# Performance work log

Measured on AMD Instinct MI355X. Metric: run time of the kernel, lower is better.

The kernel has to match this reference:

```python
import jax, jax.numpy as jnp
import numpy as np


def setup_inputs() -> dict:
    key = jax.random.key(0)
    k0, k1, k2, k3 = jax.random.split(key, 4)
    B, T, D, F, E = 4, 2048, 512, 1024, 8
    x = jax.random.normal(k0, (B, T, D), dtype=jnp.float32)
    # router weight is zero-init in the original; use small random values so top-k
    router_w = 0.02 * jax.random.normal(k1, (E, D), dtype=jnp.float32)
    router_b = jnp.zeros((E,), dtype=jnp.float32)
    w_gate_up = 0.02 * jax.random.normal(k2, (E, D, 2 * F), dtype=jnp.float32)
    w_down = 0.02 * jax.random.normal(k3, (E, F, D), dtype=jnp.float32)
    return {"x": x, "router_w": router_w, "router_b": router_b,
            "w_gate_up": w_gate_up, "w_down": w_down, "top_k": 2}


def reference(x, router_w, router_b, w_gate_up, w_down, top_k):
    B, T, D = x.shape
    E = router_w.shape[0]
    x_flat = x.reshape(-1, D)                      # [N, D]
    N = x_flat.shape[0]

    # router: softmax over experts, top-k, renormalize
    logits = x_flat @ router_w.T + router_b       # [N, E]
    probs = jax.nn.softmax(logits, axis=-1)
    top_w, top_idx = jax.lax.top_k(probs, top_k)  # [N, k]
    top_w = top_w / jnp.sum(top_w, axis=-1, keepdims=True)

    # scatter renormalized weights into a dense [N, E] combine matrix
    combine = jnp.zeros((N, E), dtype=x.dtype).at[
        jnp.arange(N)[:, None], top_idx].add(top_w)

    # per-expert SwiGLU; combine weights zero out non-selected experts, giving
    # math identical to the sort/gather/scatter dispatch in the original
    out = jnp.zeros_like(x_flat)
    for e in range(E):  # fixed small expert count, not a data-dim loop
        gate_up = x_flat @ w_gate_up[e]           # [N, 2F]
        gate, up = jnp.split(gate_up, 2, axis=-1)
        h = jax.nn.silu(gate) * up                # [N, F]
        out = out + combine[:, e:e + 1] * (h @ w_down[e])
    return out.reshape(B, T, D)
```

## Files before the change

kernel.cpp:

```cpp
#include <hip/hip_runtime.h>
#include <stdint.h>

#define N_TOK 8192
#define D_DIM 512
#define F_DIM 1024
#define E_NUM 8
#define M_SLOTS (N_TOK * 2)

typedef __bf16 bf16x8 __attribute__((ext_vector_type(8)));
typedef float f32x4 __attribute__((ext_vector_type(4)));

__device__ __forceinline__ ushort f2b(float f) {
    union { float f; unsigned u; } v; v.f = f;
    unsigned r = v.u + 0x7fffu + ((v.u >> 16) & 1u);
    return (ushort)(r >> 16);
}
__device__ __forceinline__ float b2f(ushort u) {
    union { unsigned i; float f; } v; v.i = ((unsigned)u) << 16; return v.f;
}
__device__ __forceinline__ void gload16(const void* g, void* l) {
    __builtin_amdgcn_global_load_lds(
        (const __attribute__((address_space(1))) unsigned int*)g,
        (__attribute__((address_space(3))) unsigned int*)l, 16, 0, 0);
}

__global__ __launch_bounds__(256) void transpose_all_k(const float* __restrict__ wgu,
                                                       ushort* __restrict__ wgu_t,
                                                       const float* __restrict__ wd,
                                                       ushort* __restrict__ wd_t) {
    __shared__ ushort tile[64][65];
    int b = blockIdx.x;
    const float* src; ushort* dst; int R, C, c0, r0;
    if (b < 2048) {
        int e = b >> 8, rem = b & 255;
        R = D_DIM; C = 2 * F_DIM;
        src = wgu + (size_t)e * R * C; dst = wgu_t + (size_t)e * R * C;
        c0 = (rem & 31) * 64; r0 = (rem >> 5) * 64;
    } else {
        int b2 = b - 2048;
        int e = b2 >> 7, rem = b2 & 127;
        R = F_DIM; C = D_DIM;
        src = wd + (size_t)e * R * C; dst = wd_t + (size_t)e * R * C;
        c0 = (rem & 7) * 64; r0 = (rem >> 3) * 64;
    }
#pragma unroll
    for (int i = 0; i < 4; ++i) {
        int ch = threadIdx.x + i * 256;
        int row = ch >> 4, pos = ch & 15;
        float4 v = *(const float4*)(src + (size_t)(r0 + row) * C + c0 + pos * 4);
        tile[row][pos * 4 + 0] = f2b(v.x);
        tile[row][pos * 4 + 1] = f2b(v.y);
        tile[row][pos * 4 + 2] = f2b(v.z);
        tile[row][pos * 4 + 3] = f2b(v.w);
    }
    __syncthreads();
#pragma unroll
    for (int i = 0; i < 2; ++i) {
        int ch = threadIdx.x + i * 256;
        int ocol = ch >> 3, rb = ch & 7;
        ushort tmp[8];
#pragma unroll
        for (int j = 0; j < 8; ++j) tmp[j] = tile[rb * 8 + j][ocol];
        *(uint4*)(dst + (size_t)(c0 + ocol) * R + r0 + rb * 8) = *(const uint4*)tmp;
    }
}

__global__ __launch_bounds__(256) void logits_k(const float* __restrict__ x,
                                                const float* __restrict__ rw,
                                                const float* __restrict__ rb,
                                                ushort* __restrict__ x_bf,
                                                int* __restrict__ tok_e,
                                                float* __restrict__ tok_w) {
    int lane = threadIdx.x & 63, wv = threadIdx.x >> 6;
    int t = blockIdx.x * 4 + wv;
    float4 xa = *(const float4*)(x + (size_t)t * D_DIM + lane * 8);
    float4 xb = *(const float4*)(x + (size_t)t * D_DIM + lane * 8 + 4);
    ushort u[8] = {f2b(xa.x), f2b(xa.y), f2b(xa.z), f2b(xa.w),
                   f2b(xb.x), f2b(xb.y), f2b(xb.z), f2b(xb.w)};
    *(uint4*)(x_bf + (size_t)t * D_DIM + lane * 8) = *(const uint4*)u;

    float acc[E_NUM];
#pragma unroll
    for (int e = 0; e < E_NUM; ++e) {
        float4 wa = *(const float4*)(rw + (size_t)e * D_DIM + lane * 8);
        float4 wb = *(const float4*)(rw + (size_t)e * D_DIM + lane * 8 + 4);
        float s = xa.x * wa.x + xa.y * wa.y + xa.z * wa.z + xa.w * wa.w +
                  xb.x * wb.x + xb.y * wb.y + xb.z * wb.z + xb.w * wb.w;
#pragma unroll
        for (int o = 32; o > 0; o >>= 1) s += __shfl_xor(s, o, 64);
        acc[e] = s;
    }
    if (lane == 0) {
        float l[E_NUM];
#pragma unroll
        for (int e = 0; e < E_NUM; ++e) l[e] = acc[e] + rb[e];
        int e0 = 0;
#pragma unroll
        for (int e = 1; e < E_NUM; ++e) if (l[e] > l[e0]) e0 = e;
        int e1 = (e0 == 0) ? 1 : 0;
#pragma unroll
        for (int e = 0; e < E_NUM; ++e) if (e != e0 && l[e] > l[e1]) e1 = e;
        float p1 = __expf(l[e1] - l[e0]);
        float w0 = 1.f / (1.f + p1), w1 = p1 / (1.f + p1);
        tok_e[2 * t] = e0;  tok_e[2 * t + 1] = e1;
        tok_w[2 * t] = w0;  tok_w[2 * t + 1] = w1;
    }
}

__global__ __launch_bounds__(1024) void route_k(const int* __restrict__ tok_e,
                                                int* __restrict__ ebase,
                                                int* __restrict__ row_token,
                                                int* __restrict__ tok_pos) {
    __shared__ int lcnt[E_NUM];
    __shared__ int base_s[E_NUM];
    int tid = threadIdx.x, lane = tid & 63;
    if (tid < E_NUM) lcnt[tid] = 0;
    __syncthreads();
    int ev[16], intra[16];
#pragma unroll
    for (int j = 0; j < 16; ++j) {
        int i = tid + j * 1024;
        int e = tok_e[i];
        unsigned long long m = ~0ull;
#pragma unroll
        for (int b = 0; b < 3; ++b) {
            unsigned long long vb = __ballot(((e >> b) & 1) != 0);
            m &= ((e >> b) & 1) ? vb : ~vb;
        }
        int prefix = __popcll(m & ((1ull << lane) - 1ull));
        int leader = __ffsll((unsigned long long)m) - 1;
        int bs = 0;
        if (lane == leader) bs = atomicAdd(&lcnt[e], __popcll(m));
        bs = __shfl(bs, leader, 64);
        ev[j] = e; intra[j] = bs + prefix;
    }
    __syncthreads();
    if (tid == 0) {
        int s = 0;
        for (int k = 0; k < E_NUM; ++k) { base_s[k] = s; ebase[k] = s; s += lcnt[k]; }
        ebase[E_NUM] = s;
    }
    __syncthreads();
#pragma unroll
    for (int j = 0; j < 16; ++j) {
        int i = tid + j * 1024;
        int pos = base_s[ev[j]] + intra[j];
        row_token[pos] = i >> 1;
        tok_pos[i] = pos;
    }
}

__global__ __launch_bounds__(256, 3) void gemm1_k(const ushort* __restrict__ x,
                                                  const ushort* __restrict__ wgu_t,
                                                  const int* __restrict__ ebase,
                                                  const int* __restrict__ row_token,
                                                  ushort* __restrict__ h) {
    int e = blockIdx.z;
    int base = ebase[e];
    int cnt = ebase[e + 1] - base;
    int tile0 = blockIdx.y * 128;
    if (tile0 >= cnt) return;
    int c0 = blockIdx.x * 64;

    __shared__ __align__(16) ushort smem[3 * 8192];

    int tid = threadIdx.x;
    int lane = tid & 63, wv = tid >> 6;
    int wr = wv >> 1, wc = wv & 1;

    const ushort* asrc[2];
    const ushort* bsrc[2];
#pragma unroll
    for (int i = 0; i < 2; ++i) {
        int c = tid + i * 256;
        int rp = c >> 3, s = c & 7;
        int lp = s ^ (rp & 7);
        int row = 2 * rp + (lp >> 2);
        int q = lp & 3;
        int r = tile0 + row;
        r = (r < cnt) ? r : (cnt - 1);
        int tok = row_token[base + r];
        asrc[i] = x + (size_t)tok * D_DIM + q * 8;
        int gc = (row < 64) ? (c0 + row) : (F_DIM + c0 + row - 64);
        bsrc[i] = wgu_t + ((size_t)e * (2 * F_DIM) + gc) * D_DIM + q * 8;
    }

    f32x4 accg[4][2], accu[4][2];
#pragma unroll
    for (int a = 0; a < 4; ++a)
#pragma unroll
        for (int b = 0; b < 2; ++b) {
            accg[a][b] = (f32x4){0.f, 0.f, 0.f, 0.f};
            accu[a][b] = (f32x4){0.f, 0.f, 0.f, 0.f};
        }

    int q = lane >> 4, m = lane & 15;
    int mh = m >> 1;
    int sl = (4 * (m & 1) + q) ^ (mh & 7);
    int soff = sl * 8;

    auto stage = [&](ushort* buf, int kk) {
#pragma unroll
        for (int i = 0; i < 2; ++i) {
            int c = tid + i * 256;
            gload16(asrc[i] + kk, buf + (size_t)c * 8);
            gload16(bsrc[i] + kk, buf + 4096 + (size_t)c * 8);
        }
    };
    auto compute = [&](const ushort* la_) {
        const ushort* lb_ = la_ + 4096;
        bf16x8 af[4], bg[2], bu[2];
#pragma unroll
        for (int mt = 0; mt < 4; ++mt)
            af[mt] = *(const bf16x8*)(la_ + (wr * 32 + mt * 8 + mh) * 64 + soff);
#pragma unroll
        for (int nt = 0; nt < 2; ++nt) {
            bg[nt] = *(const bf16x8*)(lb_ + (wc * 16 + nt * 8 + mh) * 64 + soff);
            bu[nt] = *(const bf16x8*)(lb_ + (32 + wc * 16 + nt * 8 + mh) * 64 + soff);
        }
#pragma unroll
        for (int mt = 0; mt < 4; ++mt)
#pragma unroll
            for (int nt = 0; nt < 2; ++nt) {
                accg[mt][nt] = __builtin_amdgcn_mfma_f32_16x16x32_bf16(af[mt], bg[nt], accg[mt][nt], 0, 0, 0);
                accu[mt][nt] = __builtin_amdgcn_mfma_f32_16x16x32_bf16(af[mt], bu[nt], accu[mt][nt], 0, 0, 0);
            }
    };

    ushort* pc = smem;
    ushort* pn = smem + 8192;
    ushort* pf = smem + 16384;

    stage(pc, 0);
    stage(pn, 32);
    asm volatile("s_waitcnt vmcnt(4) lgkmcnt(0)" ::: "memory");
    __builtin_amdgcn_s_barrier();
    __builtin_amdgcn_sched_barrier(0);

    for (int k = 64; k <= D_DIM - 32; k += 32) {
        stage(pf, k);
        compute(pc);
        asm volatile("s_waitcnt vmcnt(4) lgkmcnt(0)" ::: "memory");
        __builtin_amdgcn_s_barrier();
        __builtin_amdgcn_sched_barrier(0);
        ushort* t_ = pc; pc = pn; pn = pf; pf = t_;
    }
    compute(pc);
    asm volatile("s_waitcnt vmcnt(0) lgkmcnt(0)" ::: "memory");
    __builtin_amdgcn_s_barrier();
    __builtin_amdgcn_sched_barrier(0);
    compute(pn);

    __syncthreads();
    ushort* stg = smem;
#pragma unroll
    for (int mt = 0; mt < 4; ++mt)
#pragma unroll
        for (int nt = 0; nt < 2; ++nt) {
            int sc = wc * 32 + nt * 16 + m;
#pragma unroll
            for (int r4 = 0; r4 < 4; ++r4) {
                int rr = wr * 64 + mt * 16 + q * 4 + r4;
                float g = accg[mt][nt][r4];
                float u = accu[mt][nt][r4];
                stg[rr * 68 + sc] = f2b((g / (1.f + __expf(-g))) * u);
            }
        }
    __syncthreads();
#pragma unroll
    for (int p = 0; p < 4; ++p) {
        int c = tid + p * 256;
        int sr = c >> 3, coff = (c & 7) * 8;
        int grow = tile0 + sr;
        if (grow < cnt)
            *(uint4*)(h + (size_t)(base + grow) * F_DIM + c0 + coff) =
                *(const uint4*)(stg + sr * 68 + coff);
    }
}

__global__ __launch_bounds__(256, 3) void gemm2_k(const ushort* __restrict__ h,
                                                  const ushort* __restrict__ wd_t,
                                                  const int* __restrict__ ebase,
                                                  ushort* __restrict__ slot) {
    int e = blockIdx.z;
    int base = ebase[e];
    int cnt = ebase[e + 1] - base;
    int tile0 = blockIdx.y * 128;
    if (tile0 >= cnt) return;
    int c0 = blockIdx.x * 128;

    __shared__ __align__(16) ushort smem[3 * 8192];

    int tid = threadIdx.x;
    int lane = tid & 63, wv = tid >> 6;
    int wr = wv >> 1, wc = wv & 1;

    const ushort* asrc[2]; const ushort* bsrc[2];
#pragma unroll
    for (int i = 0; i < 2; ++i) {
        int c = tid + i * 256;
        int rp = c >> 3, s = c & 7;
        int lp = s ^ (rp & 7);
        int row = 2 * rp + (lp >> 2);
        int q = lp & 3;
        int r = tile0 + row;
        r = (r < cnt) ? r : (cnt - 1);
        asrc[i] = h + (size_t)(base + r) * F_DIM + q * 8;
        bsrc[i] = wd_t + ((size_t)e * D_DIM + c0 + row) * F_DIM + q * 8;
    }

    f32x4 acc[4][4];
#pragma unroll
    for (int a = 0; a < 4; ++a)
#pragma unroll
        for (int b = 0; b < 4; ++b) acc[a][b] = (f32x4){0.f, 0.f, 0.f, 0.f};

    int q = lane >> 4, m = lane & 15;
    int mh = m >> 1;
    int sl = (4 * (m & 1) + q) ^ (mh & 7);
    int soff = sl * 8;

    auto stage = [&](ushort* buf, int kk) {
#pragma unroll
        for (int i = 0; i < 2; ++i) {
            int c = tid + i * 256;
            gload16(asrc[i] + kk, buf + (size_t)c * 8);
            gload16(bsrc[i] + kk, buf + 4096 + (size_t)c * 8);
        }
    };
    auto compute = [&](const ushort* la_) {
        const ushort* lb_ = la_ + 4096;
        bf16x8 af[4], bb[4];
#pragma unroll
        for (int mt = 0; mt < 4; ++mt)
            af[mt] = *(const bf16x8*)(la_ + (wr * 32 + mt * 8 + mh) * 64 + soff);
#pragma unroll
        for (int nt = 0; nt < 4; ++nt)
            bb[nt] = *(const bf16x8*)(lb_ + (wc * 32 + nt * 8 + mh) * 64 + soff);
#pragma unroll
        for (int mt = 0; mt < 4; ++mt)
#pragma unroll
            for (int nt = 0; nt < 4; ++nt)
                acc[mt][nt] = __builtin_amdgcn_mfma_f32_16x16x32_bf16(af[mt], bb[nt], acc[mt][nt], 0, 0, 0);
    };

    ushort* pc = smem;
    ushort* pn = smem + 8192;
    ushort* pf = smem + 16384;

    stage(pc, 0);
    stage(pn, 32);
    asm volatile("s_waitcnt vmcnt(4) lgkmcnt(0)" ::: "memory");
    __builtin_amdgcn_s_barrier();
    __builtin_amdgcn_sched_barrier(0);

    for (int k = 64; k <= F_DIM - 32; k += 32) {
        stage(pf, k);
        compute(pc);
        asm volatile("s_waitcnt vmcnt(4) lgkmcnt(0)" ::: "memory");
        __builtin_amdgcn_s_barrier();
        __builtin_amdgcn_sched_barrier(0);
        ushort* t_ = pc; pc = pn; pn = pf; pf = t_;
    }
    compute(pc);
    asm volatile("s_waitcnt vmcnt(0) lgkmcnt(0)" ::: "memory");
    __builtin_amdgcn_s_barrier();
    __builtin_amdgcn_sched_barrier(0);
    compute(pn);

    __syncthreads();
    ushort* stg = smem;
#pragma unroll
    for (int mt = 0; mt < 4; ++mt)
#pragma unroll
        for (int nt = 0; nt < 4; ++nt) {
            int scol = wc * 64 + nt * 16 + m;
#pragma unroll
            for (int r4 = 0; r4 < 4; ++r4) {
                int rr = wr * 64 + mt * 16 + q * 4 + r4;
                stg[rr * 132 + scol] = f2b(acc[mt][nt][r4]);
            }
        }
    __syncthreads();
#pragma unroll
    for (int p = 0; p < 8; ++p) {
        int c = tid + p * 256;
        int sr = c >> 4, coff = (c & 15) * 8;
        int grow = tile0 + sr;
        if (grow < cnt)
            *(uint4*)(slot + (size_t)(base + grow) * D_DIM + c0 + coff) =
                *(const uint4*)(stg + sr * 132 + coff);
    }
}

__global__ __launch_bounds__(256) void combine_k(const ushort* __restrict__ slot,
                                                 const int* __restrict__ tok_pos,
                                                 const float* __restrict__ tok_w,
                                                 float* __restrict__ out) {
    int lane = threadIdx.x & 63, wv = threadIdx.x >> 6;
    int t = blockIdx.x * 4 + wv;
    int p0 = tok_pos[2 * t], p1 = tok_pos[2 * t + 1];
    float w0 = tok_w[2 * t], w1 = tok_w[2 * t + 1];
    uint4 s0 = *(const uint4*)(slot + (size_t)p0 * D_DIM + lane * 8);
    uint4 s1 = *(const uint4*)(slot + (size_t)p1 * D_DIM + lane * 8);
    const ushort* a = (const ushort*)&s0;
    const ushort* b = (const ushort*)&s1;
    float o[8];
#pragma unroll
    for (int j = 0; j < 8; ++j) o[j] = w0 * b2f(a[j]) + w1 * b2f(b[j]);
    float* dst = out + (size_t)t * D_DIM + lane * 8;
    *(float4*)dst = (float4){o[0], o[1], o[2], o[3]};
    *(float4*)(dst + 4) = (float4){o[4], o[5], o[6], o[7]};
}

extern "C" void kernel_launch(void* const* d_in, const int* in_sizes, int n_in,
                              void* d_out, int out_size, void* d_ws, size_t ws_size,
                              hipStream_t stream) {
    const float* x   = (const float*)d_in[0];
    const float* rw  = (const float*)d_in[1];
    const float* rb  = (const float*)d_in[2];
    const float* wgu = (const float*)d_in[3];
    const float* wd  = (const float*)d_in[4];
    float* out = (float*)d_out;

    char* ws = (char*)d_ws;
    size_t off = 0;
    auto alloc = [&](size_t bytes) -> void* {
        void* p = ws + off;
        off += (bytes + 255) & ~(size_t)255;
        return p;
    };
    ushort* wgu_t     = (ushort*)alloc((size_t)E_NUM * 2 * F_DIM * D_DIM * 2);
    ushort* wd_t      = (ushort*)alloc((size_t)E_NUM * D_DIM * F_DIM * 2);
    ushort* x_bf      = (ushort*)alloc((size_t)N_TOK * D_DIM * 2);
    ushort* hbuf      = (ushort*)alloc((size_t)M_SLOTS * F_DIM * 2);
    ushort* slot      = (ushort*)alloc((size_t)M_SLOTS * D_DIM * 2);
    int*    row_token = (int*)alloc(M_SLOTS * 4);
    int*    tok_e     = (int*)alloc(M_SLOTS * 4);
    float*  tok_w     = (float*)alloc(M_SLOTS * 4);
    int*    tok_pos   = (int*)alloc(M_SLOTS * 4);
    int*    ebase     = (int*)alloc(64);

    logits_k<<<N_TOK / 4, 256, 0, stream>>>(x, rw, rb, x_bf, tok_e, tok_w);
    transpose_all_k<<<3072, 256, 0, stream>>>(wgu, wgu_t, wd, wd_t);
    route_k<<<1, 1024, 0, stream>>>(tok_e, ebase, row_token, tok_pos);
    gemm1_k<<<dim3(16, 32, E_NUM), 256, 0, stream>>>(x_bf, wgu_t, ebase, row_token, hbuf);
    gemm2_k<<<dim3(4, 32, E_NUM), 256, 0, stream>>>(hbuf, wd_t, ebase, slot);
    combine_k<<<N_TOK / 4, 256, 0, stream>>>(slot, tok_pos, tok_w, out);
}
```

Before: 216.6 us.

## Fuse logits and transpose, parallelize routing, widen gemm1 tile, add setprio

The logits and weight-transpose kernels become one launch. The single-block route kernel is replaced by a multi-block counting pass plus a scatter pass that use global atomics. gemm1's N tile doubles to 128 columns (gate and up each), which halves the number of A reloads; LDS grows and occupancy drops to 2 blocks per CU. Both GEMMs raise wave priority around the MFMA blocks. The aim is fewer launches, no serial routing kernel, and more reuse of A in gemm1, at the cost of more registers and LDS and nondeterministic slot order.

```diff
diff --git a/kernel.cpp b/kernel.cpp
--- a/kernel.cpp
+++ b/kernel.cpp
@@ -24,20 +24,66 @@
         (__attribute__((address_space(3))) unsigned int*)l, 16, 0, 0);
 }
 
-__global__ __launch_bounds__(256) void transpose_all_k(const float* __restrict__ wgu,
-                                                       ushort* __restrict__ wgu_t,
-                                                       const float* __restrict__ wd,
-                                                       ushort* __restrict__ wd_t) {
+__global__ __launch_bounds__(256) void pre_k(const float* __restrict__ x,
+                                             const float* __restrict__ rw,
+                                             const float* __restrict__ rb,
+                                             ushort* __restrict__ x_bf,
+                                             int* __restrict__ tok_e,
+                                             float* __restrict__ tok_w,
+                                             int* __restrict__ cnt,
+                                             const float* __restrict__ wgu,
+                                             ushort* __restrict__ wgu_t,
+                                             const float* __restrict__ wd,
+                                             ushort* __restrict__ wd_t) {
     __shared__ ushort tile[64][65];
     int b = blockIdx.x;
+    if (b < N_TOK / 4) {
+        if (b == 0 && threadIdx.x < 16) cnt[threadIdx.x] = 0;
+        int lane = threadIdx.x & 63, wv = threadIdx.x >> 6;
+        int t = b * 4 + wv;
+        float4 xa = *(const float4*)(x + (size_t)t * D_DIM + lane * 8);
+        float4 xb = *(const float4*)(x + (size_t)t * D_DIM + lane * 8 + 4);
+        ushort u[8] = {f2b(xa.x), f2b(xa.y), f2b(xa.z), f2b(xa.w),
+                       f2b(xb.x), f2b(xb.y), f2b(xb.z), f2b(xb.w)};
+        *(uint4*)(x_bf + (size_t)t * D_DIM + lane * 8) = *(const uint4*)u;
+
+        float acc[E_NUM];
+#pragma unroll
+        for (int e = 0; e < E_NUM; ++e) {
+            float4 wa = *(const float4*)(rw + (size_t)e * D_DIM + lane * 8);
+            float4 wb = *(const float4*)(rw + (size_t)e * D_DIM + lane * 8 + 4);
+            float s = xa.x * wa.x + xa.y * wa.y + xa.z * wa.z + xa.w * wa.w +
+                      xb.x * wb.x + xb.y * wb.y + xb.z * wb.z + xb.w * wb.w;
+#pragma unroll
+            for (int o = 32; o > 0; o >>= 1) s += __shfl_xor(s, o, 64);
+            acc[e] = s;
+        }
+        if (lane == 0) {
+            float l[E_NUM];
+#pragma unroll
+            for (int e = 0; e < E_NUM; ++e) l[e] = acc[e] + rb[e];
+            int e0 = 0;
+#pragma unroll
+            for (int e = 1; e < E_NUM; ++e) if (l[e] > l[e0]) e0 = e;
+            int e1 = (e0 == 0) ? 1 : 0;
+#pragma unroll
+            for (int e = 0; e < E_NUM; ++e) if (e != e0 && l[e] > l[e1]) e1 = e;
+            float p1 = __expf(l[e1] - l[e0]);
+            float w0 = 1.f / (1.f + p1), w1 = p1 / (1.f + p1);
+            tok_e[2 * t] = e0;  tok_e[2 * t + 1] = e1;
+            tok_w[2 * t] = w0;  tok_w[2 * t + 1] = w1;
+        }
+        return;
+    }
+    int tb = b - N_TOK / 4;
     const float* src; ushort* dst; int R, C, c0, r0;
-    if (b < 2048) {
-        int e = b >> 8, rem = b & 255;
+    if (tb < 2048) {
+        int e = tb >> 8, rem = tb & 255;
         R = D_DIM; C = 2 * F_DIM;
         src = wgu + (size_t)e * R * C; dst = wgu_t + (size_t)e * R * C;
         c0 = (rem & 31) * 64; r0 = (rem >> 5) * 64;
     } else {
-        int b2 = b - 2048;
+        int b2 = tb - 2048;
         int e = b2 >> 7, rem = b2 & 127;
         R = F_DIM; C = D_DIM;
         src = wd + (size_t)e * R * C; dst = wd_t + (size_t)e * R * C;
@@ -57,100 +103,55 @@
 #pragma unroll
     for (int i = 0; i < 2; ++i) {
         int ch = threadIdx.x + i * 256;
-        int ocol = ch >> 3, rb = ch & 7;
+        int ocol = ch >> 3, rb_ = ch & 7;
         ushort tmp[8];
 #pragma unroll
-        for (int j = 0; j < 8; ++j) tmp[j] = tile[rb * 8 + j][ocol];
-        *(uint4*)(dst + (size_t)(c0 + ocol) * R + r0 + rb * 8) = *(const uint4*)tmp;
-    }
-}
-
-__global__ __launch_bounds__(256) void logits_k(const float* __restrict__ x,
-                                                const float* __restrict__ rw,
-                                                const float* __restrict__ rb,
-                                                ushort* __restrict__ x_bf,
-                                                int* __restrict__ tok_e,
-                                                float* __restrict__ tok_w) {
-    int lane = threadIdx.x & 63, wv = threadIdx.x >> 6;
-    int t = blockIdx.x * 4 + wv;
-    float4 xa = *(const float4*)(x + (size_t)t * D_DIM + lane * 8);
-    float4 xb = *(const float4*)(x + (size_t)t * D_DIM + lane * 8 + 4);
-    ushort u[8] = {f2b(xa.x), f2b(xa.y), f2b(xa.z), f2b(xa.w),
-                   f2b(xb.x), f2b(xb.y), f2b(xb.z), f2b(xb.w)};
-    *(uint4*)(x_bf + (size_t)t * D_DIM + lane * 8) = *(const uint4*)u;
-
-    float acc[E_NUM];
-#pragma unroll
-    for (int e = 0; e < E_NUM; ++e) {
-        float4 wa = *(const float4*)(rw + (size_t)e * D_DIM + lane * 8);
-        float4 wb = *(const float4*)(rw + (size_t)e * D_DIM + lane * 8 + 4);
-        float s = xa.x * wa.x + xa.y * wa.y + xa.z * wa.z + xa.w * wa.w +
-                  xb.x * wb.x + xb.y * wb.y + xb.z * wb.z + xb.w * wb.w;
-#pragma unroll
-        for (int o = 32; o > 0; o >>= 1) s += __shfl_xor(s, o, 64);
-        acc[e] = s;
-    }
-    if (lane == 0) {
-        float l[E_NUM];
-#pragma unroll
-        for (int e = 0; e < E_NUM; ++e) l[e] = acc[e] + rb[e];
-        int e0 = 0;
-#pragma unroll
-        for (int e = 1; e < E_NUM; ++e) if (l[e] > l[e0]) e0 = e;
-        int e1 = (e0 == 0) ? 1 : 0;
-#pragma unroll
-        for (int e = 0; e < E_NUM; ++e) if (e != e0 && l[e] > l[e1]) e1 = e;
-        float p1 = __expf(l[e1] - l[e0]);
-        float w0 = 1.f / (1.f + p1), w1 = p1 / (1.f + p1);
-        tok_e[2 * t] = e0;  tok_e[2 * t + 1] = e1;
-        tok_w[2 * t] = w0;  tok_w[2 * t + 1] = w1;
-    }
-}
-
-__global__ __launch_bounds__(1024) void route_k(const int* __restrict__ tok_e,
-                                                int* __restrict__ ebase,
-                                                int* __restrict__ row_token,
-                                                int* __restrict__ tok_pos) {
-    __shared__ int lcnt[E_NUM];
-    __shared__ int base_s[E_NUM];
-    int tid = threadIdx.x, lane = tid & 63;
+        for (int j = 0; j < 8; ++j) tmp[j] = tile[rb_ * 8 + j][ocol];
+        *(uint4*)(dst + (size_t)(c0 + ocol) * R + r0 + rb_ * 8) = *(const uint4*)tmp;
+    }
+}
+
+__global__ __launch_bounds__(256) void assign_k(const int* __restrict__ tok_e,
+                                                int* __restrict__ cnt,
+                                                int* __restrict__ rank) {
+    __shared__ int lcnt[E_NUM], lbase[E_NUM];
+    int tid = threadIdx.x;
+    int i = blockIdx.x * 256 + tid;
     if (tid < E_NUM) lcnt[tid] = 0;
     __syncthreads();
-    int ev[16], intra[16];
-#pragma unroll
-    for (int j = 0; j < 16; ++j) {
-        int i = tid + j * 1024;
-        int e = tok_e[i];
-        unsigned long long m = ~0ull;
-#pragma unroll
-        for (int b = 0; b < 3; ++b) {
-            unsigned long long vb = __ballot(((e >> b) & 1) != 0);
-            m &= ((e >> b) & 1) ? vb : ~vb;
-        }
-        int prefix = __popcll(m & ((1ull << lane) - 1ull));
-        int leader = __ffsll((unsigned long long)m) - 1;
-        int bs = 0;
-        if (lane == leader) bs = atomicAdd(&lcnt[e], __popcll(m));
-        bs = __shfl(bs, leader, 64);
-        ev[j] = e; intra[j] = bs + prefix;
-    }
-    __syncthreads();
+    int e = tok_e[i];
+    int intra = atomicAdd(&lcnt[e], 1);
+    __syncthreads();
+    if (tid < E_NUM) lbase[tid] = atomicAdd(&cnt[tid], lcnt[tid]);
+    __syncthreads();
+    rank[i] = lbase[e] + intra;
+}
+
+__global__ __launch_bounds__(256) void scatter_k(const int* __restrict__ tok_e,
+                                                 const int* __restrict__ rank,
+                                                 const int* __restrict__ cnt,
+                                                 int* __restrict__ ebase,
+                                                 int* __restrict__ row_token,
+                                                 int* __restrict__ tok_pos) {
+    __shared__ int eb[E_NUM];
+    int tid = threadIdx.x;
     if (tid == 0) {
         int s = 0;
-        for (int k = 0; k < E_NUM; ++k) { base_s[k] = s; ebase[k] = s; s += lcnt[k]; }
-        ebase[E_NUM] = s;
-    }
-    __syncthreads();
-#pragma unroll
-    for (int j = 0; j < 16; ++j) {
-        int i = tid + j * 1024;
-        int pos = base_s[ev[j]] + intra[j];
-        row_token[pos] = i >> 1;
-        tok_pos[i] = pos;
-    }
-}
-
-__global__ __launch_bounds__(256, 3) void gemm1_k(const ushort* __restrict__ x,
+        for (int k = 0; k < E_NUM; ++k) {
+            eb[k] = s;
+            if (blockIdx.x == 0) ebase[k] = s;
+            s += cnt[k];
+        }
+        if (blockIdx.x == 0) ebase[E_NUM] = s;
+    }
+    __syncthreads();
+    int i = blockIdx.x * 256 + tid;
+    int pos = eb[tok_e[i]] + rank[i];
+    row_token[pos] = i >> 1;
+    tok_pos[i] = pos;
+}
+
+__global__ __launch_bounds__(256, 2) void gemm1_k(const ushort* __restrict__ x,
                                                   const ushort* __restrict__ wgu_t,
                                                   const int* __restrict__ ebase,
                                                   const int* __restrict__ row_token,
@@ -160,36 +161,39 @@
     int cnt = ebase[e + 1] - base;
     int tile0 = blockIdx.y * 128;
     if (tile0 >= cnt) return;
-    int c0 = blockIdx.x * 64;
-
-    __shared__ __align__(16) ushort smem[3 * 8192];
+    int c0 = blockIdx.x * 128;
+
+    __shared__ __align__(16) ushort smem[3 * 12288];
 
     int tid = threadIdx.x;
     int lane = tid & 63, wv = tid >> 6;
     int wr = wv >> 1, wc = wv & 1;
 
-    const ushort* asrc[2];
-    const ushort* bsrc[2];
-#pragma unroll
-    for (int i = 0; i < 2; ++i) {
-        int c = tid + i * 256;
+    const ushort* src6[6];
+#pragma unroll
+    for (int i = 0; i < 6; ++i) {
+        int c6 = tid + i * 256;
+        int c = (c6 < 512) ? c6 : (c6 - 512);
         int rp = c >> 3, s = c & 7;
         int lp = s ^ (rp & 7);
         int row = 2 * rp + (lp >> 2);
         int q = lp & 3;
-        int r = tile0 + row;
-        r = (r < cnt) ? r : (cnt - 1);
-        int tok = row_token[base + r];
-        asrc[i] = x + (size_t)tok * D_DIM + q * 8;
-        int gc = (row < 64) ? (c0 + row) : (F_DIM + c0 + row - 64);
-        bsrc[i] = wgu_t + ((size_t)e * (2 * F_DIM) + gc) * D_DIM + q * 8;
-    }
-
-    f32x4 accg[4][2], accu[4][2];
+        if (c6 < 512) {
+            int r = tile0 + row;
+            r = (r < cnt) ? r : (cnt - 1);
+            int tok = row_token[base + r];
+            src6[i] = x + (size_t)tok * D_DIM + q * 8;
+        } else {
+            int gc = (row < 128) ? (c0 + row) : (F_DIM + c0 + row - 128);
+            src6[i] = wgu_t + ((size_t)e * (2 * F_DIM) + gc) * D_DIM + q * 8;
+        }
+    }
+
+    f32x4 accg[4][4], accu[4][4];
 #pragma unroll
     for (int a = 0; a < 4; ++a)
 #pragma unroll
-        for (int b = 0; b < 2; ++b) {
+        for (int b = 0; b < 4; ++b) {
             accg[a][b] = (f32x4){0.f, 0.f, 0.f, 0.f};
             accu[a][b] = (f32x4){0.f, 0.f, 0.f, 0.f};
         }
@@ -201,46 +205,47 @@
 
     auto stage = [&](ushort* buf, int kk) {
 #pragma unroll
-        for (int i = 0; i < 2; ++i) {
-            int c = tid + i * 256;
-            gload16(asrc[i] + kk, buf + (size_t)c * 8);
-            gload16(bsrc[i] + kk, buf + 4096 + (size_t)c * 8);
+        for (int i = 0; i < 6; ++i) {
+            int c6 = tid + i * 256;
+            gload16(src6[i] + kk, buf + (size_t)c6 * 8);
         }
     };
     auto compute = [&](const ushort* la_) {
         const ushort* lb_ = la_ + 4096;
-        bf16x8 af[4], bg[2], bu[2];
+        bf16x8 af[4], bg[4], bu[4];
 #pragma unroll
         for (int mt = 0; mt < 4; ++mt)
             af[mt] = *(const bf16x8*)(la_ + (wr * 32 + mt * 8 + mh) * 64 + soff);
 #pragma unroll
-        for (int nt = 0; nt < 2; ++nt) {
-            bg[nt] = *(const bf16x8*)(lb_ + (wc * 16 + nt * 8 + mh) * 64 + soff);
-            bu[nt] = *(const bf16x8*)(lb_ + (32 + wc * 16 + nt * 8 + mh) * 64 + soff);
-        }
+        for (int nt = 0; nt < 4; ++nt) {
+            bg[nt] = *(const bf16x8*)(lb_ + (wc * 32 + nt * 8 + mh) * 64 + soff);
+            bu[nt] = *(const bf16x8*)(lb_ + (64 + wc * 32 + nt * 8 + mh) * 64 + soff);
+        }
+        __builtin_amdgcn_s_setprio(1);
 #pragma unroll
         for (int mt = 0; mt < 4; ++mt)
 #pragma unroll
-            for (int nt = 0; nt < 2; ++nt) {
+            for (int nt = 0; nt < 4; ++nt) {
                 accg[mt][nt] = __builtin_amdgcn_mfma_f32_16x16x32_bf16(af[mt], bg[nt], accg[mt][nt], 0, 0, 0);
                 accu[mt][nt] = __builtin_amdgcn_mfma_f32_16x16x32_bf16(af[mt], bu[nt], accu[mt][nt], 0, 0, 0);
             }
+        __builtin_amdgcn_s_setprio(0);
     };
 
     ushort* pc = smem;
-    ushort* pn = smem + 8192;
-    ushort* pf = smem + 16384;
+    ushort* pn = smem + 12288;
+    ushort* pf = smem + 24576;
 
     stage(pc, 0);
     stage(pn, 32);
-    asm volatile("s_waitcnt vmcnt(4) lgkmcnt(0)" ::: "memory");
+    asm volatile("s_waitcnt vmcnt(6) lgkmcnt(0)" ::: "memory");
     __builtin_amdgcn_s_barrier();
     __builtin_amdgcn_sched_barrier(0);
 
     for (int k = 64; k <= D_DIM - 32; k += 32) {
         stage(pf, k);
         compute(pc);
-        asm volatile("s_waitcnt vmcnt(4) lgkmcnt(0)" ::: "memory");
+        asm volatile("s_waitcnt vmcnt(6) lgkmcnt(0)" ::: "memory");
         __builtin_amdgcn_s_barrier();
         __builtin_amdgcn_sched_barrier(0);
         ushort* t_ = pc; pc = pn; pn = pf; pf = t_;
@@ -256,25 +261,25 @@
 #pragma unroll
     for (int mt = 0; mt < 4; ++mt)
 #pragma unroll
-        for (int nt = 0; nt < 2; ++nt) {
-            int sc = wc * 32 + nt * 16 + m;
+        for (int nt = 0; nt < 4; ++nt) {
+            int sc = wc * 64 + nt * 16 + m;
 #pragma unroll
             for (int r4 = 0; r4 < 4; ++r4) {
                 int rr = wr * 64 + mt * 16 + q * 4 + r4;
                 float g = accg[mt][nt][r4];
                 float u = accu[mt][nt][r4];
-                stg[rr * 68 + sc] = f2b((g / (1.f + __expf(-g))) * u);
+                stg[rr * 132 + sc] = f2b((g / (1.f + __expf(-g))) * u);
             }
         }
     __syncthreads();
 #pragma unroll
-    for (int p = 0; p < 4; ++p) {
+    for (int p = 0; p < 8; ++p) {
         int c = tid + p * 256;
-        int sr = c >> 3, coff = (c & 7) * 8;
+        int sr = c >> 4, coff = (c & 15) * 8;
         int grow = tile0 + sr;
         if (grow < cnt)
             *(uint4*)(h + (size_t)(base + grow) * F_DIM + c0 + coff) =
-                *(const uint4*)(stg + sr * 68 + coff);
+                *(const uint4*)(stg + sr * 132 + coff);
     }
 }
 
@@ -337,11 +342,13 @@
 #pragma unroll
         for (int nt = 0; nt < 4; ++nt)
             bb[nt] = *(const bf16x8*)(lb_ + (wc * 32 + nt * 8 + mh) * 64 + soff);
+        __builtin_amdgcn_s_setprio(1);
 #pragma unroll
         for (int mt = 0; mt < 4; ++mt)
 #pragma unroll
             for (int nt = 0; nt < 4; ++nt)
                 acc[mt][nt] = __builtin_amdgcn_mfma_f32_16x16x32_bf16(af[mt], bb[nt], acc[mt][nt], 0, 0, 0);
+        __builtin_amdgcn_s_setprio(0);
     };
 
     ushort* pc = smem;
@@ -437,14 +444,17 @@
     ushort* slot      = (ushort*)alloc((size_t)M_SLOTS * D_DIM * 2);
     int*    row_token = (int*)alloc(M_SLOTS * 4);
     int*    tok_e     = (int*)alloc(M_SLOTS * 4);
+    int*    rankbuf   = (int*)alloc(M_SLOTS * 4);
     float*  tok_w     = (float*)alloc(M_SLOTS * 4);
     int*    tok_pos   = (int*)alloc(M_SLOTS * 4);
+    int*    cnt       = (int*)alloc(64);
     int*    ebase     = (int*)alloc(64);
 
-    logits_k<<<N_TOK / 4, 256, 0, stream>>>(x, rw, rb, x_bf, tok_e, tok_w);
-    transpose_all_k<<<3072, 256, 0, stream>>>(wgu, wgu_t, wd, wd_t);
-    route_k<<<1, 1024, 0, stream>>>(tok_e, ebase, row_token, tok_pos);
-    gemm1_k<<<dim3(16, 32, E_NUM), 256, 0, stream>>>(x_bf, wgu_t, ebase, row_token, hbuf);
+    pre_k<<<N_TOK / 4 + 3072, 256, 0, stream>>>(x, rw, rb, x_bf, tok_e, tok_w, cnt,
+                                                wgu, wgu_t, wd, wd_t);
+    assign_k<<<M_SLOTS / 256, 256, 0, stream>>>(tok_e, cnt, rankbuf);
+    scatter_k<<<M_SLOTS / 256, 256, 0, stream>>>(tok_e, rankbuf, cnt, ebase, row_token, tok_pos);
+    gemm1_k<<<dim3(8, 32, E_NUM), 256, 0, stream>>>(x_bf, wgu_t, ebase, row_token, hbuf);
     gemm2_k<<<dim3(4, 32, E_NUM), 256, 0, stream>>>(hbuf, wd_t, ebase, slot);
     combine_k<<<N_TOK / 4, 256, 0, stream>>>(slot, tok_pos, tok_w, out);
 }
```

After: 208.6 us. 1.04x faster.
